# Performance work log

Measured on AMD Instinct MI355X. Metric: run time of the kernel, lower is better.

Reference implementation:

```python
import jax, jax.numpy as jnp
import numpy as np

NEG_INF = -1e9
LEAKY_SLOPE = 0.2


def setup_inputs() -> dict:
    key = jax.random.key(0)
    k1, k2, k3, k4, k5 = jax.random.split(key, 5)
    B, N, F_in, F_out = 8, 2048, 256, 256
    x = jax.random.normal(k1, (B, N, F_in), dtype=jnp.float32)
    adj = jax.random.randint(k2, (B, N, N), 0, 2, dtype=jnp.int32)
    W = jax.random.normal(k3, (F_out, F_in), dtype=jnp.float32) * 0.05
    a_src = jax.random.normal(k4, (F_out,), dtype=jnp.float32) * 0.05
    a_dst = jax.random.normal(k5, (F_out,), dtype=jnp.float32) * 0.05
    return {"x": x, "adj": adj, "W": W, "a_src": a_src, "a_dst": a_dst}


def reference(x, adj, W, a_src, a_dst):
    # h: (B, N, F_out)
    h = jnp.einsum("bnf,of->bno", x, W)
    # a([h_i ; h_j]) == h_i @ a_src + h_j @ a_dst  (avoids O(N^2, 2F) concat)
    s_src = h @ a_src  # (B, N) score contribution of row node i
    s_dst = h @ a_dst  # (B, N) score contribution of col node j
    e = s_src[:, :, None] + s_dst[:, None, :]  # (B, N, N)
    e = jax.nn.leaky_relu(e, negative_slope=LEAKY_SLOPE)
    e = jnp.where(adj == 0, jnp.float32(NEG_INF), e)
    alpha = jax.nn.softmax(e, axis=-1)  # dropout is identity in eval mode
    h_prime = jnp.einsum("bij,bjo->bio", alpha, h)
    return h_prime
```

## Files before the change

kernel.cpp:

```cpp
#include <hip/hip_runtime.h>
#include <hip/hip_bf16.h>
#include <cstdint>
#include <cstddef>

typedef __attribute__((ext_vector_type(8))) short short8;
typedef __attribute__((ext_vector_type(4))) short short4v;
typedef __attribute__((ext_vector_type(4))) float floatx4;
typedef __attribute__((ext_vector_type(16))) float floatx16;
typedef unsigned short ushort_t;

#define LOG2E 1.44269504088896340736f

__device__ __forceinline__ unsigned short f2bf(float f) {
    unsigned u = __float_as_uint(f);
    u += 0x7FFFu + ((u >> 16) & 1u);
    return (unsigned short)(u >> 16);
}
__device__ __forceinline__ float bf2f(unsigned short s) {
    return __uint_as_float(((unsigned)s) << 16);
}

__global__ __launch_bounds__(256) void wprep(const float* __restrict__ W,
                                             ushort_t* __restrict__ Wb) {
    int t = blockIdx.x * 256 + threadIdx.x;
    float4 v = ((const float4*)W)[t];
    short4v s;
    s[0] = (short)f2bf(v.x); s[1] = (short)f2bf(v.y);
    s[2] = (short)f2bf(v.z); s[3] = (short)f2bf(v.w);
    ((short4v*)Wb)[t] = s;
}

__global__ __launch_bounds__(1024) void gemm_h(const float* __restrict__ x,
                                               const ushort_t* __restrict__ Wb,
                                               ushort_t* __restrict__ hT,
                                               const float* __restrict__ a_src,
                                               const float* __restrict__ a_dst,
                                               float* __restrict__ s_src,
                                               float* __restrict__ s_dst) {
    const int tid = threadIdx.x;
    const int w = tid >> 6, lane = tid & 63;
    const int q = lane >> 4, t16 = lane & 15;
    const int jg = w >> 2, og = w & 3;

    __shared__ ushort_t wt[256][72];
    __shared__ float sred[2][4][64];

    const int jrow = blockIdx.x * 64 + jg * 16 + t16;
    const float* xr = x + (size_t)jrow * 256 + q * 8;
    short8 af[8];
#pragma unroll
    for (int kb = 0; kb < 8; ++kb) {
        float4 v0 = *(const float4*)(xr + kb * 32);
        float4 v1 = *(const float4*)(xr + kb * 32 + 4);
        short8 a;
        a[0] = (short)f2bf(v0.x); a[1] = (short)f2bf(v0.y);
        a[2] = (short)f2bf(v0.z); a[3] = (short)f2bf(v0.w);
        a[4] = (short)f2bf(v1.x); a[5] = (short)f2bf(v1.y);
        a[6] = (short)f2bf(v1.z); a[7] = (short)f2bf(v1.w);
        af[kb] = a;
    }

    floatx4 acc[4] = {};
#pragma unroll
    for (int kp = 0; kp < 4; ++kp) {
        if (kp) __syncthreads();
#pragma unroll
        for (int r = 0; r < 2; ++r) {
            int G = tid + 1024 * r;
            int row = G >> 3, g = G & 7;
            int4 wv = *(const int4*)(Wb + (size_t)row * 256 + kp * 64 + g * 8);
            *(int4*)(&wt[row][g * 8]) = wv;
        }
        __syncthreads();
#pragma unroll
        for (int ks = 0; ks < 2; ++ks) {
#pragma unroll
            for (int ct = 0; ct < 4; ++ct) {
                short8 bf = *(const short8*)(&wt[og * 64 + ct * 16 + t16][ks * 32 + q * 8]);
                acc[ct] = __builtin_amdgcn_mfma_f32_16x16x32_bf16(af[kp * 2 + ks], bf, acc[ct], 0, 0, 0);
            }
        }
    }

    const int jbase = blockIdx.x * 64 + jg * 16 + q * 4;
    const int b = jbase >> 11, jj = jbase & 2047;
#pragma unroll
    for (int ct = 0; ct < 4; ++ct) {
        const int o = og * 64 + ct * 16 + t16;
        short4v sv;
        sv[0] = (short)f2bf(acc[ct][0]);
        sv[1] = (short)f2bf(acc[ct][1]);
        sv[2] = (short)f2bf(acc[ct][2]);
        sv[3] = (short)f2bf(acc[ct][3]);
        *(short4v*)(hT + ((size_t)b * 256 + o) * 2048 + jj) = sv;
    }

    float psv[4] = {}, pdv[4] = {};
#pragma unroll
    for (int ct = 0; ct < 4; ++ct) {
        const int o = og * 64 + ct * 16 + t16;
        float as = a_src[o], ad = a_dst[o];
#pragma unroll
        for (int r = 0; r < 4; ++r) {
            psv[r] = __fmaf_rn(acc[ct][r], as, psv[r]);
            pdv[r] = __fmaf_rn(acc[ct][r], ad, pdv[r]);
        }
    }
#pragma unroll
    for (int m = 1; m < 16; m <<= 1) {
#pragma unroll
        for (int r = 0; r < 4; ++r) {
            psv[r] += __shfl_xor(psv[r], m);
            pdv[r] += __shfl_xor(pdv[r], m);
        }
    }
    if (t16 == 0) {
#pragma unroll
        for (int r = 0; r < 4; ++r) {
            sred[0][og][jg * 16 + q * 4 + r] = psv[r];
            sred[1][og][jg * 16 + q * 4 + r] = pdv[r];
        }
    }
    __syncthreads();
    if (tid < 64) {
        float ss = sred[0][0][tid] + sred[0][1][tid] + sred[0][2][tid] + sred[0][3][tid];
        float dd = sred[1][0][tid] + sred[1][1][tid] + sred[1][2][tid] + sred[1][3][tid];
        s_src[blockIdx.x * 64 + tid] = ss;
        s_dst[blockIdx.x * 64 + tid] = dd;
    }
}

__global__ __launch_bounds__(1024) void attn(const ushort_t* __restrict__ hT,
                                             const int* __restrict__ adj,
                                             const float* __restrict__ s_src,
                                             const float* __restrict__ s_dst,
                                             float* __restrict__ out) {
    const int tid = threadIdx.x;
    const int w = tid >> 6;
    const int lane = tid & 63;
    const int l5 = lane & 31, hi = lane >> 5;
    const int b = blockIdx.x;
    const int i0 = blockIdx.y * 64;

    __shared__ ushort_t hts[2][256][40];
    __shared__ ushort_t ps[2][64][40];
    __shared__ float sdl[2048];
    __shared__ float rls[64];

    const float* sdb = s_dst + (size_t)b * 2048;
    {
        int idx = tid * 2;
        float2 v = *(const float2*)(sdb + idx);
        v.x *= LOG2E; v.y *= LOG2E;
        *(float2*)(&sdl[idx]) = v;
    }

    const int ip = w * 4 + (lane >> 4);
    const int jp = lane & 15;
    const float si = s_src[(size_t)b * 2048 + i0 + ip] * LOG2E;
    const int* adjr = adj + ((size_t)b * 2048 + i0 + ip) * 2048 + jp * 2;

    const int hrow = tid >> 2, hseg = tid & 3;
    const ushort_t* hTg = hT + ((size_t)b * 256 + hrow) * 2048 + hseg * 8;

    const int osub = (w & 7) * 32, ih = (w >> 3) * 32;

    floatx16 acc = {};
    float lsum = 0.f;
    int4 hreg;
    int2 a2;

    hreg = *(const int4*)(hTg);
    a2 = *(const int2*)(adjr);
    __syncthreads();

    for (int c = 0; c < 64; ++c) {
        const int buf = c & 1;
        *(int4*)(&hts[buf][hrow][hseg * 8]) = hreg;
        int2 ac = a2;
        if (c < 63) {
            hreg = *(const int4*)(hTg + (c + 1) * 32);
            a2 = *(const int2*)(adjr + (size_t)(c + 1) * 32);
        }
        {
            float2 sd = *(const float2*)(&sdl[c * 32 + jp * 2]);
            float t0 = si + sd.x;
            float t1 = si + sd.y;
            float l0 = fmaxf(t0, 0.2f * t0);
            float l1 = fmaxf(t1, 0.2f * t1);
            float p0 = __builtin_amdgcn_exp2f(l0);
            float p1 = __builtin_amdgcn_exp2f(l1);
            p0 = (ac.x != 0) ? p0 : 0.0f;
            p1 = (ac.y != 0) ? p1 : 0.0f;
            unsigned short u0 = f2bf(p0);
            unsigned short u1 = f2bf(p1);
            lsum += bf2f(u0) + bf2f(u1);
            *(unsigned*)(&ps[buf][ip][jp * 2]) = (unsigned)u0 | ((unsigned)u1 << 16);
        }
        __syncthreads();
#pragma unroll
        for (int ks = 0; ks < 2; ++ks) {
            short8 afr = *(const short8*)(&hts[buf][osub + l5][ks * 16 + hi * 8]);
            short8 bfr = *(const short8*)(&ps[buf][ih + l5][ks * 16 + hi * 8]);
            acc = __builtin_amdgcn_mfma_f32_32x32x16_bf16(afr, bfr, acc, 0, 0, 0);
        }
    }

#pragma unroll
    for (int m = 1; m < 16; m <<= 1) lsum += __shfl_xor(lsum, m);
    if (jp == 0) rls[ip] = lsum;
    __syncthreads();

    {
        const int i = ih + l5;
        const float s = rls[i];
        const float rl = (s > 0.f) ? 1.0f / s : 0.0f;
        float* orow = out + ((size_t)b * 2048 + i0 + i) * 256 + osub;
#pragma unroll
        for (int rq = 0; rq < 4; ++rq) {
            floatx4 v;
            v[0] = acc[rq * 4 + 0] * rl;
            v[1] = acc[rq * 4 + 1] * rl;
            v[2] = acc[rq * 4 + 2] * rl;
            v[3] = acc[rq * 4 + 3] * rl;
            *(floatx4*)(orow + rq * 8 + hi * 4) = v;
        }
    }
}

extern "C" void kernel_launch(void* const* d_in, const int* in_sizes, int n_in,
                              void* d_out, int out_size, void* d_ws, size_t ws_size,
                              hipStream_t stream) {
    const float* x     = (const float*)d_in[0];
    const int*   adj   = (const int*)d_in[1];
    const float* W     = (const float*)d_in[2];
    const float* a_src = (const float*)d_in[3];
    const float* a_dst = (const float*)d_in[4];
    float* out = (float*)d_out;

    char* ws = (char*)d_ws;
    ushort_t* hT = (ushort_t*)ws;
    float* s_src = (float*)(ws + (size_t)8 * 1024 * 1024);
    float* s_dst = s_src + 16384;
    ushort_t* Wb = (ushort_t*)(s_dst + 16384);

    wprep<<<64, 256, 0, stream>>>(W, Wb);
    gemm_h<<<256, 1024, 0, stream>>>(x, Wb, hT, a_src, a_dst, s_src, s_dst);
    attn<<<dim3(8, 32), 1024, 0, stream>>>(hT, adj, s_src, s_dst, out);
}
```

Baseline: 249.0 us.

## Bit-pack adjacency in GEMM kernel and rewrite attention kernel without shared memory

Drops the separate W conversion kernel and converts W and x to bf16 inside the GEMM using LDS staging. The GEMM kernel also packs the int32 adjacency matrix into 64-bit bitmasks and writes h in an MFMA-fragment-ordered layout. The attention kernel then uses smaller 256-thread blocks that load fragments straight from global memory into registers with double buffering, with no LDS or barriers. Softmax row sums are now reduced within a wave. The 64 MB adjacency read moves into the GEMM kernel, and the attention grid changes to 512 blocks.

```diff
diff --git a/kernel.cpp b/kernel.cpp
--- a/kernel.cpp
+++ b/kernel.cpp
@@ -8,6 +8,7 @@
 typedef __attribute__((ext_vector_type(4))) float floatx4;
 typedef __attribute__((ext_vector_type(16))) float floatx16;
 typedef unsigned short ushort_t;
+typedef unsigned long long u64_t;
 
 #define LOG2E 1.44269504088896340736f
 
@@ -20,45 +21,23 @@
     return __uint_as_float(((unsigned)s) << 16);
 }
 
-__global__ __launch_bounds__(256) void wprep(const float* __restrict__ W,
-                                             ushort_t* __restrict__ Wb) {
-    int t = blockIdx.x * 256 + threadIdx.x;
-    float4 v = ((const float4*)W)[t];
-    short4v s;
-    s[0] = (short)f2bf(v.x); s[1] = (short)f2bf(v.y);
-    s[2] = (short)f2bf(v.z); s[3] = (short)f2bf(v.w);
-    ((short4v*)Wb)[t] = s;
-}
-
 __global__ __launch_bounds__(1024) void gemm_h(const float* __restrict__ x,
-                                               const ushort_t* __restrict__ Wb,
-                                               ushort_t* __restrict__ hT,
+                                               const float* __restrict__ W,
+                                               const int* __restrict__ adj,
+                                               ushort_t* __restrict__ hTf,
                                                const float* __restrict__ a_src,
                                                const float* __restrict__ a_dst,
                                                float* __restrict__ s_src,
-                                               float* __restrict__ s_dst) {
+                                               float* __restrict__ s_dst,
+                                               u64_t* __restrict__ adjb) {
     const int tid = threadIdx.x;
     const int w = tid >> 6, lane = tid & 63;
-    const int q = lane >> 4, t16 = lane & 15;
+    const int q = (lane >> 4) & 3, t16 = lane & 15;
     const int jg = w >> 2, og = w & 3;
 
     __shared__ ushort_t wt[256][72];
+    __shared__ ushort_t xs[64][72];
     __shared__ float sred[2][4][64];
-
-    const int jrow = blockIdx.x * 64 + jg * 16 + t16;
-    const float* xr = x + (size_t)jrow * 256 + q * 8;
-    short8 af[8];
-#pragma unroll
-    for (int kb = 0; kb < 8; ++kb) {
-        float4 v0 = *(const float4*)(xr + kb * 32);
-        float4 v1 = *(const float4*)(xr + kb * 32 + 4);
-        short8 a;
-        a[0] = (short)f2bf(v0.x); a[1] = (short)f2bf(v0.y);
-        a[2] = (short)f2bf(v0.z); a[3] = (short)f2bf(v0.w);
-        a[4] = (short)f2bf(v1.x); a[5] = (short)f2bf(v1.y);
-        a[6] = (short)f2bf(v1.z); a[7] = (short)f2bf(v1.w);
-        af[kb] = a;
-    }
 
     floatx4 acc[4] = {};
 #pragma unroll
@@ -68,22 +47,39 @@
         for (int r = 0; r < 2; ++r) {
             int G = tid + 1024 * r;
             int row = G >> 3, g = G & 7;
-            int4 wv = *(const int4*)(Wb + (size_t)row * 256 + kp * 64 + g * 8);
-            *(int4*)(&wt[row][g * 8]) = wv;
+            const float* wsrc = W + (size_t)row * 256 + kp * 64 + g * 8;
+            float4 f0 = *(const float4*)(wsrc);
+            float4 f1 = *(const float4*)(wsrc + 4);
+            short8 wv;
+            wv[0] = (short)f2bf(f0.x); wv[1] = (short)f2bf(f0.y);
+            wv[2] = (short)f2bf(f0.z); wv[3] = (short)f2bf(f0.w);
+            wv[4] = (short)f2bf(f1.x); wv[5] = (short)f2bf(f1.y);
+            wv[6] = (short)f2bf(f1.z); wv[7] = (short)f2bf(f1.w);
+            *(short8*)(&wt[row][g * 8]) = wv;
+        }
+        {
+            int row = tid >> 4, kc = (tid & 15) * 4;
+            float4 xv = *(const float4*)(x + (size_t)(blockIdx.x * 64 + row) * 256 + kp * 64 + kc);
+            short4v s;
+            s[0] = (short)f2bf(xv.x); s[1] = (short)f2bf(xv.y);
+            s[2] = (short)f2bf(xv.z); s[3] = (short)f2bf(xv.w);
+            *(short4v*)(&xs[row][kc]) = s;
         }
         __syncthreads();
 #pragma unroll
         for (int ks = 0; ks < 2; ++ks) {
+            short8 af = *(const short8*)(&xs[jg * 16 + t16][ks * 32 + q * 8]);
 #pragma unroll
             for (int ct = 0; ct < 4; ++ct) {
                 short8 bf = *(const short8*)(&wt[og * 64 + ct * 16 + t16][ks * 32 + q * 8]);
-                acc[ct] = __builtin_amdgcn_mfma_f32_16x16x32_bf16(af[kp * 2 + ks], bf, acc[ct], 0, 0, 0);
+                acc[ct] = __builtin_amdgcn_mfma_f32_16x16x32_bf16(af, bf, acc[ct], 0, 0, 0);
             }
         }
     }
 
     const int jbase = blockIdx.x * 64 + jg * 16 + q * 4;
     const int b = jbase >> 11, jj = jbase & 2047;
+    const int c = jj >> 5, ksb = (jj >> 4) & 1, hib = (jj >> 3) & 1, e0 = jj & 7;
 #pragma unroll
     for (int ct = 0; ct < 4; ++ct) {
         const int o = og * 64 + ct * 16 + t16;
@@ -92,7 +88,9 @@
         sv[1] = (short)f2bf(acc[ct][1]);
         sv[2] = (short)f2bf(acc[ct][2]);
         sv[3] = (short)f2bf(acc[ct][3]);
-        *(short4v*)(hT + ((size_t)b * 256 + o) * 2048 + jj) = sv;
+        size_t eidx = (((((size_t)b * 8 + (o >> 5)) * 64 + c) * 2 + ksb) * 64
+                       + hib * 32 + (o & 31)) * 8 + e0;
+        *(short4v*)(hTf + eidx) = sv;
     }
 
     float psv[4] = {}, pdv[4] = {};
@@ -125,106 +123,145 @@
     if (tid < 64) {
         float ss = sred[0][0][tid] + sred[0][1][tid] + sred[0][2][tid] + sred[0][3][tid];
         float dd = sred[1][0][tid] + sred[1][1][tid] + sred[1][2][tid] + sred[1][3][tid];
-        s_src[blockIdx.x * 64 + tid] = ss;
-        s_dst[blockIdx.x * 64 + tid] = dd;
-    }
-}
-
-__global__ __launch_bounds__(1024) void attn(const ushort_t* __restrict__ hT,
-                                             const int* __restrict__ adj,
-                                             const float* __restrict__ s_src,
-                                             const float* __restrict__ s_dst,
-                                             float* __restrict__ out) {
+        s_src[blockIdx.x * 64 + tid] = ss * LOG2E;
+        s_dst[blockIdx.x * 64 + tid] = dd * LOG2E;
+    }
+
+    {
+        const int g16 = lane >> 4, l16 = lane & 15;
+#pragma unroll
+        for (int rr = 0; rr < 4; ++rr) {
+            const int row = blockIdx.x * 64 + w * 4 + rr;
+            const int* ap = adj + (size_t)row * 2048;
+#pragma unroll 4
+            for (int s = 0; s < 8; ++s) {
+                int4 v = *(const int4*)(ap + s * 256 + lane * 4);
+                unsigned nib = (v.x != 0 ? 1u : 0u) | (v.y != 0 ? 2u : 0u) |
+                               (v.z != 0 ? 4u : 0u) | (v.w != 0 ? 8u : 0u);
+                u64_t val = (u64_t)nib << (l16 * 4);
+                val |= __shfl_xor(val, 1);
+                val |= __shfl_xor(val, 2);
+                val |= __shfl_xor(val, 4);
+                val |= __shfl_xor(val, 8);
+                if (l16 == 0) adjb[(size_t)row * 32 + s * 4 + g16] = val;
+            }
+        }
+    }
+}
+
+#define PEL(sv, mw, bit, pk, idx)                                            \
+    {   float t_ = si + (sv);                                                \
+        float l_ = fmaxf(t_, 0.2f * t_);                                     \
+        float p_ = __builtin_amdgcn_exp2f(l_);                               \
+        p_ = ((mw >> (bit)) & 1u) ? p_ : 0.0f;                               \
+        unsigned short u_ = f2bf(p_);                                        \
+        lsum += bf2f(u_);                                                    \
+        pk[idx] = (short)u_; }
+
+#define PROD(W32, S0, S1, S2, S3)                                            \
+    {   unsigned mA = ((W32) >> (hi * 8)) & 0xffu;                           \
+        unsigned mB = ((W32) >> (hi * 8 + 16)) & 0xffu;                      \
+        PEL(S0.x, mA, 0, pa, 0) PEL(S0.y, mA, 1, pa, 1)                      \
+        PEL(S0.z, mA, 2, pa, 2) PEL(S0.w, mA, 3, pa, 3)                      \
+        PEL(S1.x, mA, 4, pa, 4) PEL(S1.y, mA, 5, pa, 5)                      \
+        PEL(S1.z, mA, 6, pa, 6) PEL(S1.w, mA, 7, pa, 7)                      \
+        PEL(S2.x, mB, 0, pb, 0) PEL(S2.y, mB, 1, pb, 1)                      \
+        PEL(S2.z, mB, 2, pb, 2) PEL(S2.w, mB, 3, pb, 3)                      \
+        PEL(S3.x, mB, 4, pb, 4) PEL(S3.y, mB, 5, pb, 5)                      \
+        PEL(S3.z, mB, 6, pb, 6) PEL(S3.w, mB, 7, pb, 7) }
+
+#define LOADFRAG(F00, F01, F10, F11, cc)                                     \
+    F00 = *(const short8*)(fb + (size_t)(cc) * 1024);                        \
+    F01 = *(const short8*)(fb + (size_t)(cc) * 1024 + 512);                  \
+    F10 = *(const short8*)(fb + 65536 + (size_t)(cc) * 1024);                \
+    F11 = *(const short8*)(fb + 65536 + (size_t)(cc) * 1024 + 512);
+
+#define LOADSD(S0, S1, S2, S3, cc)                                           \
+    S0 = *(const float4*)(sdb + (cc) * 32 + hi * 8);                         \
+    S1 = *(const float4*)(sdb + (cc) * 32 + hi * 8 + 4);                     \
+    S2 = *(const float4*)(sdb + (cc) * 32 + hi * 8 + 16);                    \
+    S3 = *(const float4*)(sdb + (cc) * 32 + hi * 8 + 20);
+
+#define MM(F00, F01, F10, F11)                                               \
+    acc0 = __builtin_amdgcn_mfma_f32_32x32x16_bf16(F00, pa, acc0, 0, 0, 0);  \
+    acc0 = __builtin_amdgcn_mfma_f32_32x32x16_bf16(F01, pb, acc0, 0, 0, 0);  \
+    acc1 = __builtin_amdgcn_mfma_f32_32x32x16_bf16(F10, pa, acc1, 0, 0, 0);  \
+    acc1 = __builtin_amdgcn_mfma_f32_32x32x16_bf16(F11, pb, acc1, 0, 0, 0);
+
+__global__ __launch_bounds__(256) void attn(const ushort_t* __restrict__ hTf,
+                                            const u64_t* __restrict__ adjb,
+                                            const float* __restrict__ s_src,
+                                            const float* __restrict__ s_dst,
+                                            float* __restrict__ out) {
     const int tid = threadIdx.x;
-    const int w = tid >> 6;
+    const int ot = tid >> 6;
     const int lane = tid & 63;
     const int l5 = lane & 31, hi = lane >> 5;
-    const int b = blockIdx.x;
-    const int i0 = blockIdx.y * 64;
-
-    __shared__ ushort_t hts[2][256][40];
-    __shared__ ushort_t ps[2][64][40];
-    __shared__ float sdl[2048];
-    __shared__ float rls[64];
-
+    const int bid = blockIdx.x;
+    const int b = bid & 7;
+    const int i0 = (bid >> 3) * 32;
+
+    const float si = s_src[b * 2048 + i0 + l5];
     const float* sdb = s_dst + (size_t)b * 2048;
-    {
-        int idx = tid * 2;
-        float2 v = *(const float2*)(sdb + idx);
-        v.x *= LOG2E; v.y *= LOG2E;
-        *(float2*)(&sdl[idx]) = v;
-    }
-
-    const int ip = w * 4 + (lane >> 4);
-    const int jp = lane & 15;
-    const float si = s_src[(size_t)b * 2048 + i0 + ip] * LOG2E;
-    const int* adjr = adj + ((size_t)b * 2048 + i0 + ip) * 2048 + jp * 2;
-
-    const int hrow = tid >> 2, hseg = tid & 3;
-    const ushort_t* hTg = hT + ((size_t)b * 256 + hrow) * 2048 + hseg * 8;
-
-    const int osub = (w & 7) * 32, ih = (w >> 3) * 32;
-
-    floatx16 acc = {};
+    const u64_t* amr = adjb + ((size_t)b * 2048 + i0 + l5) * 32;
+    const ushort_t* fb = hTf + (size_t)(b * 8 + ot * 2) * 65536 + lane * 8;
+
+    floatx16 acc0 = {}, acc1 = {};
     float lsum = 0.f;
-    int4 hreg;
-    int2 a2;
-
-    hreg = *(const int4*)(hTg);
-    a2 = *(const int2*)(adjr);
-    __syncthreads();
-
-    for (int c = 0; c < 64; ++c) {
-        const int buf = c & 1;
-        *(int4*)(&hts[buf][hrow][hseg * 8]) = hreg;
-        int2 ac = a2;
-        if (c < 63) {
-            hreg = *(const int4*)(hTg + (c + 1) * 32);
-            a2 = *(const int2*)(adjr + (size_t)(c + 1) * 32);
-        }
-        {
-            float2 sd = *(const float2*)(&sdl[c * 32 + jp * 2]);
-            float t0 = si + sd.x;
-            float t1 = si + sd.y;
-            float l0 = fmaxf(t0, 0.2f * t0);
-            float l1 = fmaxf(t1, 0.2f * t1);
-            float p0 = __builtin_amdgcn_exp2f(l0);
-            float p1 = __builtin_amdgcn_exp2f(l1);
-            p0 = (ac.x != 0) ? p0 : 0.0f;
-            p1 = (ac.y != 0) ? p1 : 0.0f;
-            unsigned short u0 = f2bf(p0);
-            unsigned short u1 = f2bf(p1);
-            lsum += bf2f(u0) + bf2f(u1);
-            *(unsigned*)(&ps[buf][ip][jp * 2]) = (unsigned)u0 | ((unsigned)u1 << 16);
-        }
-        __syncthreads();
-#pragma unroll
-        for (int ks = 0; ks < 2; ++ks) {
-            short8 afr = *(const short8*)(&hts[buf][osub + l5][ks * 16 + hi * 8]);
-            short8 bfr = *(const short8*)(&ps[buf][ih + l5][ks * 16 + hi * 8]);
-            acc = __builtin_amdgcn_mfma_f32_32x32x16_bf16(afr, bfr, acc, 0, 0, 0);
-        }
-    }
-
-#pragma unroll
-    for (int m = 1; m < 16; m <<= 1) lsum += __shfl_xor(lsum, m);
-    if (jp == 0) rls[ip] = lsum;
-    __syncthreads();
-
-    {
-        const int i = ih + l5;
-        const float s = rls[i];
-        const float rl = (s > 0.f) ? 1.0f / s : 0.0f;
-        float* orow = out + ((size_t)b * 2048 + i0 + i) * 256 + osub;
-#pragma unroll
-        for (int rq = 0; rq < 4; ++rq) {
-            floatx4 v;
-            v[0] = acc[rq * 4 + 0] * rl;
-            v[1] = acc[rq * 4 + 1] * rl;
-            v[2] = acc[rq * 4 + 2] * rl;
-            v[3] = acc[rq * 4 + 3] * rl;
-            *(floatx4*)(orow + rq * 8 + hi * 4) = v;
-        }
+    short8 fE00, fE01, fE10, fE11, fO00, fO01, fO10, fO11, pa, pb;
+    float4 sE0, sE1, sE2, sE3, sO0, sO1, sO2, sO3;
+    u64_t mkC, mkN;
+
+    mkC = amr[0];
+    LOADFRAG(fE00, fE01, fE10, fE11, 0)
+    LOADSD(sE0, sE1, sE2, sE3, 0)
+    LOADFRAG(fO00, fO01, fO10, fO11, 1)
+    LOADSD(sO0, sO1, sO2, sO3, 1)
+
+#pragma unroll 1
+    for (int t = 0; t < 32; ++t) {
+        const int c = t * 2;
+        mkN = amr[(t < 31) ? t + 1 : 31];
+        {
+            unsigned w32 = (unsigned)mkC;
+            PROD(w32, sE0, sE1, sE2, sE3)
+            MM(fE00, fE01, fE10, fE11)
+        }
+        {
+            const int nc = (c + 2 < 64) ? c + 2 : 62;
+            LOADFRAG(fE00, fE01, fE10, fE11, nc)
+            LOADSD(sE0, sE1, sE2, sE3, nc)
+        }
+        {
+            unsigned w32 = (unsigned)(mkC >> 32);
+            PROD(w32, sO0, sO1, sO2, sO3)
+            MM(fO00, fO01, fO10, fO11)
+        }
+        {
+            const int nc = (c + 3 < 64) ? c + 3 : 63;
+            LOADFRAG(fO00, fO01, fO10, fO11, nc)
+            LOADSD(sO0, sO1, sO2, sO3, nc)
+        }
+        mkC = mkN;
+    }
+
+    lsum += __shfl_xor(lsum, 32);
+    const float rl = (lsum > 0.f) ? 1.0f / lsum : 0.0f;
+
+    float* orow = out + ((size_t)b * 2048 + i0 + l5) * 256 + ot * 64;
+#pragma unroll
+    for (int rq = 0; rq < 4; ++rq) {
+        floatx4 v;
+        v[0] = acc0[rq * 4 + 0] * rl;
+        v[1] = acc0[rq * 4 + 1] * rl;
+        v[2] = acc0[rq * 4 + 2] * rl;
+        v[3] = acc0[rq * 4 + 3] * rl;
+        *(floatx4*)(orow + rq * 8 + hi * 4) = v;
+        v[0] = acc1[rq * 4 + 0] * rl;
+        v[1] = acc1[rq * 4 + 1] * rl;
+        v[2] = acc1[rq * 4 + 2] * rl;
+        v[3] = acc1[rq * 4 + 3] * rl;
+        *(floatx4*)(orow + 32 + rq * 8 + hi * 4) = v;
     }
 }
 
@@ -239,12 +276,11 @@
     float* out = (float*)d_out;
 
     char* ws = (char*)d_ws;
-    ushort_t* hT = (ushort_t*)ws;
+    ushort_t* hTf = (ushort_t*)ws;
     float* s_src = (float*)(ws + (size_t)8 * 1024 * 1024);
     float* s_dst = s_src + 16384;
-    ushort_t* Wb = (ushort_t*)(s_dst + 16384);
-
-    wprep<<<64, 256, 0, stream>>>(W, Wb);
-    gemm_h<<<256, 1024, 0, stream>>>(x, Wb, hT, a_src, a_dst, s_src, s_dst);
-    attn<<<dim3(8, 32), 1024, 0, stream>>>(hT, adj, s_src, s_dst, out);
-}
+    u64_t* adjb  = (u64_t*)(s_dst + 16384);
+
+    gemm_h<<<256, 1024, 0, stream>>>(x, W, adj, hTf, a_src, a_dst, s_src, s_dst, adjb);
+    attn<<<512, 256, 0, stream>>>(hTf, adjb, s_src, s_dst, out);
+}
```

After: 277.8 us. +11.6%, slower.
